# Optimization experiments

Hardware: AMD Instinct MI355X
Metric: run time of the kernel (lower is better)

Reference implementation:

```python
import jax, jax.numpy as jnp
import numpy as np

N = 100000      # nodes
E = 1600000     # edges (avg degree 16)
D_IN = 256
H = 128         # hidden_dim
D_OUT = 64
BN_EPS = 1e-5


def setup_inputs() -> dict:
    key = jax.random.key(0)
    ks = jax.random.split(key, 16)
    s = 0.05  # small init scale
    x = jax.random.normal(ks[0], (N, D_IN), jnp.float32)
    edge_index = jax.random.randint(ks[1], (2, E), 0, N)
    inp = {
        "x": x,
        "edge_index": edge_index,
        "w_in": jax.random.normal(ks[2], (D_IN, H), jnp.float32) * s,
        "b_in": jnp.zeros((H,), jnp.float32),
        # SAGEConv layer 1: lin_l (neighbors, with bias) + lin_r (self, no bias)
        "w_l1": jax.random.normal(ks[3], (H, H), jnp.float32) * s,
        "b_l1": jnp.zeros((H,), jnp.float32),
        "w_r1": jax.random.normal(ks[4], (H, H), jnp.float32) * s,
        "g1": jnp.ones((H,), jnp.float32),
        "be1": jnp.zeros((H,), jnp.float32),
        # SAGEConv layer 2
        "w_l2": jax.random.normal(ks[5], (H, H), jnp.float32) * s,
        "b_l2": jnp.zeros((H,), jnp.float32),
        "w_r2": jax.random.normal(ks[6], (H, H), jnp.float32) * s,
        "g2": jnp.ones((H,), jnp.float32),
        "be2": jnp.zeros((H,), jnp.float32),
        "w_out": jax.random.normal(ks[7], (H, D_OUT), jnp.float32) * s,
        "b_out": jnp.zeros((D_OUT,), jnp.float32),
    }
    return inp


def _sage_conv(x, src, dst, w_l, b_l, w_r):
    # gather messages from source nodes, mean-aggregate at target nodes
    msgs = x[src]                                           # [E, H]
    agg = jax.ops.segment_sum(msgs, dst, num_segments=N)    # [N, H]
    deg = jax.ops.segment_sum(jnp.ones((src.shape[0], 1), x.dtype), dst,
                              num_segments=N)               # [N, 1]
    mean = agg / jnp.maximum(deg, 1.0)
    return mean @ w_l + b_l + x @ w_r


def _bn_eval(h, gamma, beta):
    # BatchNorm1d in eval mode: running_mean=0, running_var=1
    return h * (gamma / jnp.sqrt(1.0 + BN_EPS)) + beta


def reference(x, edge_index, w_in, b_in,
              w_l1, b_l1, w_r1, g1, be1,
              w_l2, b_l2, w_r2, g2, be2,
              w_out, b_out):
    src, dst = edge_index[0], edge_index[1]
    h = jax.nn.relu(x @ w_in + b_in)                         # [N, H]
    h = _sage_conv(h, src, dst, w_l1, b_l1, w_r1)
    h = jax.nn.relu(_bn_eval(h, g1, be1))                    # dropout off (eval)
    h = _sage_conv(h, src, dst, w_l2, b_l2, w_r2)
    h = jax.nn.relu(_bn_eval(h, g2, be2))
    return h @ w_out + b_out                                 # [N, D_OUT]
```

## Files before the change

kernel.cpp:

```cpp
#include <hip/hip_runtime.h>

#define DIN 256
#define H   128
#define DOUT 64

#define EPI_RELU 0
#define EPI_BN   1
#define EPI_NONE 2

#define BKT_SHIFT 7
#define BKT_NODES 128
#define BKT_CAP   4096

typedef __attribute__((ext_vector_type(8))) short bf16x8;
typedef __attribute__((ext_vector_type(4))) float f32x4;

__device__ inline unsigned short f2bf(float f) {
  union { float f; unsigned u; } v; v.f = f;
  unsigned u = v.u;
  u += 0x7FFFu + ((u >> 16) & 1u);
  return (unsigned short)(u >> 16);
}
__device__ inline float bf2f(unsigned u16) {
  union { unsigned u; float f; } v; v.u = u16 << 16;
  return v.f;
}

#define FILL_TPB 1024
#define FILL_EPT 16
#define FILL_EPB (FILL_TPB * FILL_EPT)

__global__ __launch_bounds__(FILL_TPB) void bucket_fill(
    const int* __restrict__ src, const int* __restrict__ dst,
    int* __restrict__ bcur, unsigned* __restrict__ bedges,
    int nbkt, int e) {
  __shared__ int hist[1024];
  int tid = threadIdx.x;
  int base = blockIdx.x * FILL_EPB;
  for (int i = tid; i < nbkt; i += FILL_TPB) hist[i] = 0;
  __syncthreads();

  int es[FILL_EPT], ed[FILL_EPT];
#pragma unroll
  for (int j = 0; j < FILL_EPT; ++j) {
    int i = base + j * FILL_TPB + tid;
    if (i < e) {
      es[j] = src[i];
      ed[j] = dst[i];
      atomicAdd(&hist[ed[j] >> BKT_SHIFT], 1);
    } else {
      es[j] = -1; ed[j] = 0;
    }
  }
  __syncthreads();
  for (int b = tid; b < nbkt; b += FILL_TPB) {
    int cnt = hist[b];
    hist[b] = cnt ? atomicAdd(&bcur[b], cnt) : 0;
  }
  __syncthreads();
#pragma unroll
  for (int j = 0; j < FILL_EPT; ++j) {
    if (es[j] >= 0) {
      int b = ed[j] >> BKT_SHIFT;
      int p = atomicAdd(&hist[b], 1);
      if (p < BKT_CAP)
        bedges[(size_t)b * BKT_CAP + p] =
            (unsigned)es[j] | ((unsigned)(ed[j] & (BKT_NODES - 1)) << 17);
    }
  }
}

__global__ __launch_bounds__(256) void bucket_sort(
    const int* __restrict__ bcur, const unsigned* __restrict__ bedges,
    int* __restrict__ csr, int* __restrict__ row_beg, int* __restrict__ deg,
    int n) {
  __shared__ unsigned rec[BKT_CAP];
  __shared__ int srcs[BKT_CAP];
  __shared__ int hist[BKT_NODES];
  __shared__ int cursor[BKT_NODES];
  int tid = threadIdx.x;
  int b = blockIdx.x;
  int cnt = bcur[b];
  if (cnt > BKT_CAP) cnt = BKT_CAP;
  const unsigned* eb = bedges + (size_t)b * BKT_CAP;

  if (tid < BKT_NODES) hist[tid] = 0;
  __syncthreads();
  for (int i = tid; i < cnt; i += 256) {
    unsigned r = eb[i];
    rec[i] = r;
    atomicAdd(&hist[(r >> 17) & 127], 1);
  }
  __syncthreads();
  int myc = (tid < BKT_NODES) ? hist[tid] : 0;
#pragma unroll
  for (int off = 1; off < BKT_NODES; off <<= 1) {
    int v = 0;
    if (tid < BKT_NODES && tid >= off) v = hist[tid - off];
    __syncthreads();
    if (tid < BKT_NODES) hist[tid] += v;
    __syncthreads();
  }
  if (tid < BKT_NODES) {
    int start = hist[tid] - myc;
    cursor[tid] = start;
    int node = b * BKT_NODES + tid;
    if (node < n) {
      row_beg[node] = b * BKT_CAP + start;
      deg[node] = myc;
    }
  }
  __syncthreads();
  for (int i = tid; i < cnt; i += 256) {
    unsigned r = rec[i];
    int p = atomicAdd(&cursor[(r >> 17) & 127], 1);
    srcs[p] = (int)(r & 0x1FFFFu);
  }
  __syncthreads();
  for (int i = tid; i < cnt; i += 256)
    csr[(size_t)b * BKT_CAP + i] = srcs[i];
}

__global__ __launch_bounds__(256) void agg_kernel(const unsigned* __restrict__ h,
                                                  const int* __restrict__ row_beg,
                                                  const int* __restrict__ deg,
                                                  const int* __restrict__ csr,
                                                  unsigned* __restrict__ mean, int n) {
  int node = (int)((blockIdx.x * blockDim.x + threadIdx.x) >> 6);
  if (node >= n) return;
  int lane = threadIdx.x & 63;
  int beg = row_beg[node], d = deg[node];
  float ax = 0.f, ay = 0.f;
  for (int j0 = 0; j0 < d; j0 += 64) {
    int cnt = min(64, d - j0);
    int li = j0 + (lane < cnt ? lane : cnt - 1);
    int sv = csr[beg + li];
    int j = 0;
    for (; j + 8 <= cnt; j += 8) {
      unsigned v[8];
#pragma unroll
      for (int q = 0; q < 8; ++q) {
        int s = __shfl(sv, j + q);
        v[q] = h[(size_t)s * (H / 2) + lane];
      }
#pragma unroll
      for (int q = 0; q < 8; ++q) {
        ax += bf2f(v[q] & 0xffffu);
        ay += bf2f(v[q] >> 16);
      }
    }
    for (; j < cnt; ++j) {
      int s = __shfl(sv, j);
      unsigned v = h[(size_t)s * (H / 2) + lane];
      ax += bf2f(v & 0xffffu);
      ay += bf2f(v >> 16);
    }
  }
  float invd = 1.f / (float)(d > 0 ? d : 1);
  mean[(size_t)node * (H / 2) + lane] =
      (unsigned)f2bf(ax * invd) | ((unsigned)f2bf(ay * invd) << 16);
}

__global__ __launch_bounds__(256) void prep_w(
    const float* __restrict__ w_in, const float* __restrict__ w_l1,
    const float* __restrict__ w_r1, const float* __restrict__ w_l2,
    const float* __restrict__ w_r2, const float* __restrict__ w_out,
    unsigned short* __restrict__ t_in, unsigned short* __restrict__ t_l1,
    unsigned short* __restrict__ t_r1, unsigned short* __restrict__ t_l2,
    unsigned short* __restrict__ t_r2, unsigned short* __restrict__ t_out) {
  int i = blockIdx.x * 256 + threadIdx.x;
  const float* s; unsigned short* d; int K, M, off;
  if (i < 32768)       { s = w_in;  d = t_in;  K = 256; M = 128; off = i; }
  else if (i < 49152)  { s = w_l1;  d = t_l1;  K = 128; M = 128; off = i - 32768; }
  else if (i < 65536)  { s = w_r1;  d = t_r1;  K = 128; M = 128; off = i - 49152; }
  else if (i < 81920)  { s = w_l2;  d = t_l2;  K = 128; M = 128; off = i - 65536; }
  else if (i < 98304)  { s = w_r2;  d = t_r2;  K = 128; M = 128; off = i - 81920; }
  else if (i < 106496) { s = w_out; d = t_out; K = 128; M = 64;  off = i - 98304; }
  else return;
  int m = off / K, k = off % K;
  d[off] = f2bf(s[(size_t)k * M + m]);
}

template <int NPH, int KOFF2, int AK, int M, int EPI, bool AFP32, bool OUTF32>
__global__ __launch_bounds__(256) void gemm_mfma(
    const void* __restrict__ A1, const void* __restrict__ A2,
    const unsigned short* __restrict__ W1, const unsigned short* __restrict__ W2,
    const float* __restrict__ bias, const float* __restrict__ gamma,
    const float* __restrict__ beta, void* __restrict__ Cv, int n) {
  constexpr int KP = 136;
  constexpr int NT = M / 16;
  __shared__ __align__(16) unsigned short Bs[M * KP];

  int tid = threadIdx.x, lane = tid & 63, wave = tid >> 6;
  int m16 = lane & 15, quad = lane >> 4;
  int row0 = blockIdx.x * 128;

  f32x4 acc[2][NT];
#pragma unroll
  for (int rt = 0; rt < 2; ++rt)
#pragma unroll
    for (int t = 0; t < NT; ++t) acc[rt][t] = (f32x4){0.f, 0.f, 0.f, 0.f};

  int rowa[2];
#pragma unroll
  for (int rt = 0; rt < 2; ++rt) {
    int r = row0 + wave * 32 + rt * 16 + m16;
    rowa[rt] = (r < n) ? r : (n - 1);
  }

  bf16x8 af[NPH][2][4];
  if constexpr (!AFP32) {
#pragma unroll
    for (int ph = 0; ph < NPH; ++ph) {
      const unsigned short* A = (const unsigned short*)(ph ? A2 : A1);
      const int koff = ph ? KOFF2 : 0;
#pragma unroll
      for (int rt = 0; rt < 2; ++rt)
#pragma unroll
        for (int kt = 0; kt < 4; ++kt)
          af[ph][rt][kt] = *(const bf16x8*)(A + (size_t)rowa[rt] * AK + koff +
                                            kt * 32 + quad * 8);
    }
  }

#pragma unroll
  for (int ph = 0; ph < NPH; ++ph) {
    const unsigned short* W = ph ? W2 : W1;
    const int koff = ph ? KOFF2 : 0;
    if (ph) __syncthreads();

    if constexpr (AFP32) {
      const float* A = (const float*)(ph ? A2 : A1);
      float4 raw[2][4][2];
#pragma unroll
      for (int rt = 0; rt < 2; ++rt)
#pragma unroll
        for (int kt = 0; kt < 4; ++kt) {
          const float* ap = A + (size_t)rowa[rt] * AK + koff + kt * 32 + quad * 8;
          raw[rt][kt][0] = *(const float4*)ap;
          raw[rt][kt][1] = *(const float4*)(ap + 4);
        }
#pragma unroll
      for (int rt = 0; rt < 2; ++rt)
#pragma unroll
        for (int kt = 0; kt < 4; ++kt) {
          union { bf16x8 v; unsigned u[4]; } p;
          float4 v0 = raw[rt][kt][0], v1 = raw[rt][kt][1];
          p.u[0] = (unsigned)f2bf(v0.x) | ((unsigned)f2bf(v0.y) << 16);
          p.u[1] = (unsigned)f2bf(v0.z) | ((unsigned)f2bf(v0.w) << 16);
          p.u[2] = (unsigned)f2bf(v1.x) | ((unsigned)f2bf(v1.y) << 16);
          p.u[3] = (unsigned)f2bf(v1.z) | ((unsigned)f2bf(v1.w) << 16);
          af[ph][rt][kt] = p.v;
        }
    }

    for (int i = tid; i < M * 16; i += 256) {
      int r = i >> 4, c = i & 15;
      *(uint4*)&Bs[r * KP + c * 8] = *(const uint4*)&W[(size_t)r * AK + koff + c * 8];
    }
    __syncthreads();
#pragma unroll
    for (int kt = 0; kt < 4; ++kt) {
#pragma unroll
      for (int t = 0; t < NT; ++t) {
        bf16x8 bfr = *(const bf16x8*)&Bs[(t * 16 + m16) * KP + kt * 32 + quad * 8];
        acc[0][t] = __builtin_amdgcn_mfma_f32_16x16x32_bf16(af[ph][0][kt], bfr,
                                                            acc[0][t], 0, 0, 0);
        acc[1][t] = __builtin_amdgcn_mfma_f32_16x16x32_bf16(af[ph][1][kt], bfr,
                                                            acc[1][t], 0, 0, 0);
      }
    }
  }

  const float inv_std = rsqrtf(1.f + 1e-5f);
#pragma unroll
  for (int t = 0; t < NT; ++t) {
    int col = t * 16 + m16;
    float bv = bias[col];
    float sc = 1.f, bt2 = 0.f;
    if constexpr (EPI == EPI_BN) {
      sc = gamma[col] * inv_std;
      bt2 = beta[col];
    }
#pragma unroll
    for (int rt = 0; rt < 2; ++rt) {
#pragma unroll
      for (int r = 0; r < 4; ++r) {
        int row = row0 + wave * 32 + rt * 16 + quad * 4 + r;
        if (row < n) {
          float v = acc[rt][t][r] + bv;
          if constexpr (EPI == EPI_BN) v = fmaxf(v * sc + bt2, 0.f);
          else if constexpr (EPI == EPI_RELU) v = fmaxf(v, 0.f);
          if constexpr (OUTF32)
            ((float*)Cv)[(size_t)row * M + col] = v;
          else
            ((unsigned short*)Cv)[(size_t)row * M + col] = f2bf(v);
        }
      }
    }
  }
}

extern "C" void kernel_launch(void* const* d_in, const int* in_sizes, int n_in,
                              void* d_out, int out_size, void* d_ws, size_t ws_size,
                              hipStream_t stream) {
  const float* x     = (const float*)d_in[0];
  const int*   ei    = (const int*)d_in[1];
  const float* w_in  = (const float*)d_in[2];
  const float* b_in  = (const float*)d_in[3];
  const float* w_l1  = (const float*)d_in[4];
  const float* b_l1  = (const float*)d_in[5];
  const float* w_r1  = (const float*)d_in[6];
  const float* g1    = (const float*)d_in[7];
  const float* be1   = (const float*)d_in[8];
  const float* w_l2  = (const float*)d_in[9];
  const float* b_l2  = (const float*)d_in[10];
  const float* w_r2  = (const float*)d_in[11];
  const float* g2    = (const float*)d_in[12];
  const float* be2   = (const float*)d_in[13];
  const float* w_out = (const float*)d_in[14];
  const float* b_out = (const float*)d_in[15];
  float* out = (float*)d_out;

  int N = in_sizes[0] / DIN;
  int E = in_sizes[1] / 2;
  const int* src = ei;
  const int* dst = ei + E;
  int nbkt = (N + BKT_NODES - 1) / BKT_NODES;

  char* ws = (char*)d_ws;
  size_t off = 0;
  auto alloc = [&](size_t bytes) -> char* {
    char* p = ws + off;
    off += (bytes + 255) & ~(size_t)255;
    return p;
  };
  unsigned short* buf0 = (unsigned short*)alloc((size_t)N * H * 2);
  unsigned short* buf1 = (unsigned short*)alloc((size_t)N * H * 2);
  unsigned short* buf2 = (unsigned short*)alloc((size_t)N * H * 2);
  int* bcur        = (int*)alloc((size_t)nbkt * 4);
  unsigned* bedges = (unsigned*)alloc((size_t)nbkt * BKT_CAP * 4);
  int* csr         = (int*)alloc((size_t)nbkt * BKT_CAP * 4);
  int* row_beg     = (int*)alloc((size_t)N * 4);
  int* deg         = (int*)alloc((size_t)N * 4);
  unsigned short* t_in  = (unsigned short*)alloc(32768 * 2);
  unsigned short* t_l1  = (unsigned short*)alloc(16384 * 2);
  unsigned short* t_r1  = (unsigned short*)alloc(16384 * 2);
  unsigned short* t_l2  = (unsigned short*)alloc(16384 * 2);
  unsigned short* t_r2  = (unsigned short*)alloc(16384 * 2);
  unsigned short* t_out = (unsigned short*)alloc(8192 * 2);
  (void)ws_size;

  hipMemsetAsync(bcur, 0, (size_t)nbkt * 4, stream);
  bucket_fill<<<(E + FILL_EPB - 1) / FILL_EPB, FILL_TPB, 0, stream>>>(
      src, dst, bcur, bedges, nbkt, E);
  bucket_sort<<<nbkt, 256, 0, stream>>>(bcur, bedges, csr, row_beg, deg, N);
  prep_w<<<(106496 + 255) / 256, 256, 0, stream>>>(
      w_in, w_l1, w_r1, w_l2, w_r2, w_out, t_in, t_l1, t_r1, t_l2, t_r2, t_out);

  int gblocks = (N + 127) / 128;
  int ablocks = (N + 3) / 4;

  gemm_mfma<2, 128, 256, 128, EPI_RELU, true, false><<<gblocks, 256, 0, stream>>>(
      x, x, t_in, t_in, b_in, nullptr, nullptr, buf0, N);
  agg_kernel<<<ablocks, 256, 0, stream>>>((const unsigned*)buf0, row_beg, deg,
                                          csr, (unsigned*)buf1, N);
  gemm_mfma<2, 0, 128, 128, EPI_BN, false, false><<<gblocks, 256, 0, stream>>>(
      buf1, buf0, t_l1, t_r1, b_l1, g1, be1, buf2, N);
  agg_kernel<<<ablocks, 256, 0, stream>>>((const unsigned*)buf2, row_beg, deg,
                                          csr, (unsigned*)buf0, N);
  gemm_mfma<2, 0, 128, 128, EPI_BN, false, false><<<gblocks, 256, 0, stream>>>(
      buf0, buf2, t_l2, t_r2, b_l2, g2, be2, buf1, N);
  gemm_mfma<1, 0, 128, 64, EPI_NONE, false, true><<<gblocks, 256, 0, stream>>>(
      buf1, buf1, t_out, t_out, b_out, nullptr, nullptr, out, N);
}
```

Baseline: 466.3 us.

## Stage GEMM A tiles through swizzled LDS with coalesced loads and smaller row tiles

The MFMA GEMM now cooperatively loads A rows into shared memory with row-contiguous coalesced 16-byte loads and an XOR-style rotated (swizzled) layout, rather than each lane gathering strided fragments straight from global memory. B also uses the rotated layout instead of padding. Each block covers 64 rows instead of 128, with one 16-row tile per wave, which doubles the grid and halves the accumulators per wave. The goal is better global coalescing and occupancy, at the cost of extra LDS traffic, an extra barrier dependency, and more redundant per-block weight loads.

```diff
diff --git a/kernel.cpp b/kernel.cpp
--- a/kernel.cpp
+++ b/kernel.cpp
@@ -181,93 +181,76 @@
   d[off] = f2bf(s[(size_t)k * M + m]);
 }
 
-template <int NPH, int KOFF2, int AK, int M, int EPI, bool AFP32, bool OUTF32>
+template <int NPH, int KOFF2, int AKA, int AKW, int M, int EPI, bool AFP32, bool OUTF32>
 __global__ __launch_bounds__(256) void gemm_mfma(
     const void* __restrict__ A1, const void* __restrict__ A2,
     const unsigned short* __restrict__ W1, const unsigned short* __restrict__ W2,
     const float* __restrict__ bias, const float* __restrict__ gamma,
     const float* __restrict__ beta, void* __restrict__ Cv, int n) {
-  constexpr int KP = 136;
   constexpr int NT = M / 16;
-  __shared__ __align__(16) unsigned short Bs[M * KP];
+  __shared__ __align__(16) unsigned short As[64 * 128];
+  __shared__ __align__(16) unsigned short Bs[M * 128];
 
   int tid = threadIdx.x, lane = tid & 63, wave = tid >> 6;
   int m16 = lane & 15, quad = lane >> 4;
-  int row0 = blockIdx.x * 128;
-
-  f32x4 acc[2][NT];
-#pragma unroll
-  for (int rt = 0; rt < 2; ++rt)
-#pragma unroll
-    for (int t = 0; t < NT; ++t) acc[rt][t] = (f32x4){0.f, 0.f, 0.f, 0.f};
-
-  int rowa[2];
-#pragma unroll
-  for (int rt = 0; rt < 2; ++rt) {
-    int r = row0 + wave * 32 + rt * 16 + m16;
-    rowa[rt] = (r < n) ? r : (n - 1);
-  }
-
-  bf16x8 af[NPH][2][4];
-  if constexpr (!AFP32) {
-#pragma unroll
-    for (int ph = 0; ph < NPH; ++ph) {
-      const unsigned short* A = (const unsigned short*)(ph ? A2 : A1);
-      const int koff = ph ? KOFF2 : 0;
-#pragma unroll
-      for (int rt = 0; rt < 2; ++rt)
-#pragma unroll
-        for (int kt = 0; kt < 4; ++kt)
-          af[ph][rt][kt] = *(const bf16x8*)(A + (size_t)rowa[rt] * AK + koff +
-                                            kt * 32 + quad * 8);
-    }
-  }
+  int row0 = blockIdx.x * 64;
+  int sr = lane >> 4;
+  int sc = lane & 15;
+
+  f32x4 acc[NT];
+#pragma unroll
+  for (int t = 0; t < NT; ++t) acc[t] = (f32x4){0.f, 0.f, 0.f, 0.f};
 
 #pragma unroll
   for (int ph = 0; ph < NPH; ++ph) {
+    const void* A_ = ph ? A2 : A1;
     const unsigned short* W = ph ? W2 : W1;
     const int koff = ph ? KOFF2 : 0;
     if (ph) __syncthreads();
 
-    if constexpr (AFP32) {
-      const float* A = (const float*)(ph ? A2 : A1);
-      float4 raw[2][4][2];
-#pragma unroll
-      for (int rt = 0; rt < 2; ++rt)
-#pragma unroll
-        for (int kt = 0; kt < 4; ++kt) {
-          const float* ap = A + (size_t)rowa[rt] * AK + koff + kt * 32 + quad * 8;
-          raw[rt][kt][0] = *(const float4*)ap;
-          raw[rt][kt][1] = *(const float4*)(ap + 4);
-        }
-#pragma unroll
-      for (int rt = 0; rt < 2; ++rt)
-#pragma unroll
-        for (int kt = 0; kt < 4; ++kt) {
-          union { bf16x8 v; unsigned u[4]; } p;
-          float4 v0 = raw[rt][kt][0], v1 = raw[rt][kt][1];
-          p.u[0] = (unsigned)f2bf(v0.x) | ((unsigned)f2bf(v0.y) << 16);
-          p.u[1] = (unsigned)f2bf(v0.z) | ((unsigned)f2bf(v0.w) << 16);
-          p.u[2] = (unsigned)f2bf(v1.x) | ((unsigned)f2bf(v1.y) << 16);
-          p.u[3] = (unsigned)f2bf(v1.z) | ((unsigned)f2bf(v1.w) << 16);
-          af[ph][rt][kt] = p.v;
-        }
-    }
-
-    for (int i = tid; i < M * 16; i += 256) {
-      int r = i >> 4, c = i & 15;
-      *(uint4*)&Bs[r * KP + c * 8] = *(const uint4*)&W[(size_t)r * AK + koff + c * 8];
+    if constexpr (!AFP32) {
+#pragma unroll
+      for (int g = 0; g < 4; ++g) {
+        int lr = wave * 16 + g * 4 + sr;
+        int grow = row0 + lr; if (grow >= n) grow = n - 1;
+        uint4 v = *(const uint4*)((const unsigned short*)A_ +
+                                  (size_t)grow * AKA + koff + sc * 8);
+        *(uint4*)&As[lr * 128 + ((sc + lr) & 15) * 8] = v;
+      }
+    } else {
+      int sr2 = lane >> 5;
+      int c32 = lane & 31;
+#pragma unroll
+      for (int g = 0; g < 8; ++g) {
+        int lr = wave * 16 + g * 2 + sr2;
+        int grow = row0 + lr; if (grow >= n) grow = n - 1;
+        float4 v = *(const float4*)((const float*)A_ +
+                                    (size_t)grow * AKA + koff + c32 * 4);
+        unsigned p0 = (unsigned)f2bf(v.x) | ((unsigned)f2bf(v.y) << 16);
+        unsigned p1 = (unsigned)f2bf(v.z) | ((unsigned)f2bf(v.w) << 16);
+        int ch = c32 >> 1;
+        *(uint2*)&As[lr * 128 + ((ch + lr) & 15) * 8 + (c32 & 1) * 4] =
+            make_uint2(p0, p1);
+      }
+    }
+#pragma unroll
+    for (int g = 0; g < M / 16; ++g) {
+      int br = wave * (M / 4) + g * 4 + sr;
+      uint4 v = *(const uint4*)(W + (size_t)br * AKW + koff + sc * 8);
+      *(uint4*)&Bs[br * 128 + ((sc + br) & 15) * 8] = v;
     }
     __syncthreads();
+
+    int lrme = wave * 16 + m16;
 #pragma unroll
     for (int kt = 0; kt < 4; ++kt) {
+      int ch = kt * 4 + quad;
+      bf16x8 a = *(const bf16x8*)&As[lrme * 128 + ((ch + lrme) & 15) * 8];
 #pragma unroll
       for (int t = 0; t < NT; ++t) {
-        bf16x8 bfr = *(const bf16x8*)&Bs[(t * 16 + m16) * KP + kt * 32 + quad * 8];
-        acc[0][t] = __builtin_amdgcn_mfma_f32_16x16x32_bf16(af[ph][0][kt], bfr,
-                                                            acc[0][t], 0, 0, 0);
-        acc[1][t] = __builtin_amdgcn_mfma_f32_16x16x32_bf16(af[ph][1][kt], bfr,
-                                                            acc[1][t], 0, 0, 0);
+        int brow = t * 16 + m16;
+        bf16x8 b = *(const bf16x8*)&Bs[brow * 128 + ((ch + brow) & 15) * 8];
+        acc[t] = __builtin_amdgcn_mfma_f32_16x16x32_bf16(a, b, acc[t], 0, 0, 0);
       }
     }
   }
@@ -277,25 +260,22 @@
   for (int t = 0; t < NT; ++t) {
     int col = t * 16 + m16;
     float bv = bias[col];
-    float sc = 1.f, bt2 = 0.f;
+    float sc2 = 1.f, bt2 = 0.f;
     if constexpr (EPI == EPI_BN) {
-      sc = gamma[col] * inv_std;
+      sc2 = gamma[col] * inv_std;
       bt2 = beta[col];
     }
 #pragma unroll
-    for (int rt = 0; rt < 2; ++rt) {
-#pragma unroll
-      for (int r = 0; r < 4; ++r) {
-        int row = row0 + wave * 32 + rt * 16 + quad * 4 + r;
-        if (row < n) {
-          float v = acc[rt][t][r] + bv;
-          if constexpr (EPI == EPI_BN) v = fmaxf(v * sc + bt2, 0.f);
-          else if constexpr (EPI == EPI_RELU) v = fmaxf(v, 0.f);
-          if constexpr (OUTF32)
-            ((float*)Cv)[(size_t)row * M + col] = v;
-          else
-            ((unsigned short*)Cv)[(size_t)row * M + col] = f2bf(v);
-        }
+    for (int r = 0; r < 4; ++r) {
+      int row = row0 + wave * 16 + quad * 4 + r;
+      if (row < n) {
+        float v = acc[t][r] + bv;
+        if constexpr (EPI == EPI_BN) v = fmaxf(v * sc2 + bt2, 0.f);
+        else if constexpr (EPI == EPI_RELU) v = fmaxf(v, 0.f);
+        if constexpr (OUTF32)
+          ((float*)Cv)[(size_t)row * M + col] = v;
+        else
+          ((unsigned short*)Cv)[(size_t)row * M + col] = f2bf(v);
       }
     }
   }
@@ -358,19 +338,19 @@
   prep_w<<<(106496 + 255) / 256, 256, 0, stream>>>(
       w_in, w_l1, w_r1, w_l2, w_r2, w_out, t_in, t_l1, t_r1, t_l2, t_r2, t_out);
 
-  int gblocks = (N + 127) / 128;
+  int gblocks = (N + 63) / 64;
   int ablocks = (N + 3) / 4;
 
-  gemm_mfma<2, 128, 256, 128, EPI_RELU, true, false><<<gblocks, 256, 0, stream>>>(
+  gemm_mfma<2, 128, 256, 256, 128, EPI_RELU, true, false><<<gblocks, 256, 0, stream>>>(
       x, x, t_in, t_in, b_in, nullptr, nullptr, buf0, N);
   agg_kernel<<<ablocks, 256, 0, stream>>>((const unsigned*)buf0, row_beg, deg,
                                           csr, (unsigned*)buf1, N);
-  gemm_mfma<2, 0, 128, 128, EPI_BN, false, false><<<gblocks, 256, 0, stream>>>(
+  gemm_mfma<2, 0, 128, 128, 128, EPI_BN, false, false><<<gblocks, 256, 0, stream>>>(
       buf1, buf0, t_l1, t_r1, b_l1, g1, be1, buf2, N);
   agg_kernel<<<ablocks, 256, 0, stream>>>((const unsigned*)buf2, row_beg, deg,
                                           csr, (unsigned*)buf0, N);
-  gemm_mfma<2, 0, 128, 128, EPI_BN, false, false><<<gblocks, 256, 0, stream>>>(
+  gemm_mfma<2, 0, 128, 128, 128, EPI_BN, false, false><<<gblocks, 256, 0, stream>>>(
       buf0, buf2, t_l2, t_r2, b_l2, g2, be2, buf1, N);
-  gemm_mfma<1, 0, 128, 64, EPI_NONE, false, true><<<gblocks, 256, 0, stream>>>(
+  gemm_mfma<1, 0, 128, 128, 64, EPI_NONE, false, true><<<gblocks, 256, 0, stream>>>(
       buf1, buf1, t_out, t_out, b_out, nullptr, nullptr, out, N);
 }
```

After: 429.9 us. 7.8% less time.
